# Performance work log

Measured on AMD Instinct MI355X. Metric: run time of the kernel, lower is better.

The kernel has to match this reference:

```python
import jax, jax.numpy as jnp
import numpy as np

N_NODES = 50000
N_EDGES = 400000


def setup_inputs() -> dict:
    key = jax.random.key(0)
    k1, k2, k3, k4 = jax.random.split(key, 4)
    in_feat = jax.random.normal(k1, (2, 64, 4, N_NODES), dtype=jnp.float32)
    src = jax.random.randint(k2, (N_EDGES,), 0, N_NODES, dtype=jnp.int32)
    dst = jax.random.randint(k3, (N_EDGES,), 0, N_NODES, dtype=jnp.int32)
    W = jax.random.normal(k4, (64, 64), dtype=jnp.float32) * (1.0 / 8.0)
    b = jnp.zeros((64,), dtype=jnp.float32)
    return {"in_feat": in_feat, "src": src, "dst": dst, "W": W, "b": b}


def reference(in_feat, src, dst, W, b):
    # in_feat: (B, h, T, N). Net permutation [3,1,2,0] then [0,3,2,1] == [3,0,2,1]
    x = jnp.transpose(in_feat, (3, 0, 2, 1))  # (N, B, T, h) -- node-major for GraphConv
    N = x.shape[0]
    ones_e = jnp.ones(src.shape[0], dtype=x.dtype)
    deg_out = jnp.clip(jax.ops.segment_sum(ones_e, src, num_segments=N), 1.0)
    deg_in = jnp.clip(jax.ops.segment_sum(ones_e, dst, num_segments=N), 1.0)
    # DGL GraphConv, norm='both', in_feats == out_feats -> aggregate then matmul
    x = x * jax.lax.rsqrt(deg_out)[:, None, None, None]
    agg = jax.ops.segment_sum(x[src], dst, num_segments=N)  # (N, B, T, h)
    agg = agg * jax.lax.rsqrt(deg_in)[:, None, None, None]
    h = jnp.einsum('nbth,hf->nbtf', agg, W) + b
    h = jax.nn.relu(h)
    # inverse permutation [0,3,2,1] then [3,1,2,0] == transpose(h, (1,3,2,0))
    out = jnp.transpose(h, (1, 3, 2, 0))  # (B, h, T, N)
    return jax.nn.relu(out)
```

## Files before the change

kernel.cpp:

```cpp
#include <hip/hip_runtime.h>
#include <hip/hip_fp16.h>


typedef _Float16 half8 __attribute__((ext_vector_type(8)));
typedef float f32x4 __attribute__((ext_vector_type(4)));

extern "C" __global__ void k_deg(const int* __restrict__ src, const int* __restrict__ dst,
                                 int* __restrict__ deg_out, int* __restrict__ deg_in, int E) {
  int e = blockIdx.x * blockDim.x + threadIdx.x;
  if (e < E) {
    atomicAdd(&deg_out[src[e]], 1);
    atomicAdd(&deg_in[dst[e]], 1);
  }
}

extern "C" __global__ __launch_bounds__(256) void k_scan1(const int* __restrict__ deg_in,
                                                          const int* __restrict__ deg_out,
                                                          int* __restrict__ bsum,
                                                          float* __restrict__ rs_out,
                                                          float* __restrict__ rs_in, int N) {
  __shared__ int red[256];
  int tid = threadIdx.x;
  int i = blockIdx.x * 256 + tid;
  int di = (i < N) ? deg_in[i] : 0;
  red[tid] = di;
  if (i < N) {
    int a = deg_out[i] > 1 ? deg_out[i] : 1;
    int b = di > 1 ? di : 1;
    rs_out[i] = rsqrtf((float)a);
    rs_in[i]  = rsqrtf((float)b);
  }
  __syncthreads();
  #pragma unroll
  for (int off = 128; off > 0; off >>= 1) {
    if (tid < off) red[tid] += red[tid + off];
    __syncthreads();
  }
  if (tid == 0) bsum[blockIdx.x] = red[0];
}

extern "C" __global__ __launch_bounds__(256) void k_scan3(const int* __restrict__ deg,
                                                          const int* __restrict__ bsum,
                                                          int* __restrict__ offs,
                                                          int* __restrict__ cursor,
                                                          int M, int N) {
  __shared__ int sc[256];
  __shared__ int bs[256];
  int tid = threadIdx.x;

  int bv = (tid < M) ? bsum[tid] : 0;
  bs[tid] = bv;
  __syncthreads();
  #pragma unroll
  for (int off = 1; off < 256; off <<= 1) {
    int t = bs[tid];
    if (tid >= off) t += bs[tid - off];
    __syncthreads();
    bs[tid] = t;
    __syncthreads();
  }
  int boff = (blockIdx.x > 0) ? bs[blockIdx.x - 1] : 0;
  if (blockIdx.x == 0 && tid == 0) offs[N] = bs[255];

  int i = blockIdx.x * 256 + tid;
  int v = (i < N) ? deg[i] : 0;
  sc[tid] = v;
  __syncthreads();
  #pragma unroll
  for (int off = 1; off < 256; off <<= 1) {
    int t = sc[tid];
    if (tid >= off) t += sc[tid - off];
    __syncthreads();
    sc[tid] = t;
    __syncthreads();
  }
  if (i < N) {
    int o = boff + sc[tid] - v;
    offs[i] = o;
    cursor[i] = o;
  }
}

extern "C" __global__ void k_scatter(const int* __restrict__ src, const int* __restrict__ dst,
                                     int* __restrict__ cursor,
                                     int* __restrict__ csr_src, int E) {
  int e = blockIdx.x * blockDim.x + threadIdx.x;
  if (e < E) {
    int pos = atomicAdd(&cursor[dst[e]], 1);
    csr_src[pos] = src[e];
  }
}

extern "C" __global__ __launch_bounds__(128) void k_transform(
    const float* __restrict__ in_feat, const float* __restrict__ W,
    const float* __restrict__ rs_out, __half* __restrict__ y, int N) {
  __shared__ __half ytile[16][264];
  int tid = threadIdx.x;
  int wave = tid >> 6, l = tid & 63;
  int col = l & 15;
  int kg  = l >> 4;
  int n0 = blockIdx.x * 16;
  int btbase = blockIdx.y * 4 + wave * 2;

  half8 wf[4][2];
  #pragma unroll
  for (int ft = 0; ft < 4; ++ft)
    #pragma unroll
    for (int ks = 0; ks < 2; ++ks)
      #pragma unroll
      for (int j = 0; j < 8; ++j)
        wf[ft][ks][j] = (_Float16)W[(ks * 32 + kg * 8 + j) * 64 + ft * 16 + col];

  int nA = n0 + col;
  bool okA = (nA < N);
  float rs = okA ? rs_out[nA] : 0.0f;
  size_t hs = (size_t)4 * (size_t)N;

  float c0[8], c1[8], nx0[8], nx1[8];
  {
    int bt = btbase, b = bt >> 2, t = bt & 3;
    const float* xp = in_feat + (size_t)(b * 256 + t) * (size_t)N + nA;
    #pragma unroll
    for (int j = 0; j < 8; ++j) c0[j] = okA ? xp[(size_t)(kg * 8 + j) * hs] : 0.0f;
    #pragma unroll
    for (int j = 0; j < 8; ++j) c1[j] = okA ? xp[(size_t)(32 + kg * 8 + j) * hs] : 0.0f;
  }

  #pragma unroll
  for (int p = 0; p < 2; ++p) {
    if (p == 0) {
      int bt = btbase + 1, b = bt >> 2, t = bt & 3;
      const float* xp = in_feat + (size_t)(b * 256 + t) * (size_t)N + nA;
      #pragma unroll
      for (int j = 0; j < 8; ++j) nx0[j] = okA ? xp[(size_t)(kg * 8 + j) * hs] : 0.0f;
      #pragma unroll
      for (int j = 0; j < 8; ++j) nx1[j] = okA ? xp[(size_t)(32 + kg * 8 + j) * hs] : 0.0f;
    }
    int btloc = wave * 2 + p;

    half8 a0, a1;
    #pragma unroll
    for (int j = 0; j < 8; ++j) {
      a0[j] = (_Float16)(c0[j] * rs);
      a1[j] = (_Float16)(c1[j] * rs);
    }

    #pragma unroll
    for (int ft = 0; ft < 4; ++ft) {
      f32x4 acc = {0.f, 0.f, 0.f, 0.f};
      acc = __builtin_amdgcn_mfma_f32_16x16x32_f16(a0, wf[ft][0], acc, 0, 0, 0);
      acc = __builtin_amdgcn_mfma_f32_16x16x32_f16(a1, wf[ft][1], acc, 0, 0, 0);
      #pragma unroll
      for (int r = 0; r < 4; ++r)
        ytile[kg * 4 + r][btloc * 64 + ft * 16 + col] = __float2half(acc[r]);
    }

    if (p == 0) {
      #pragma unroll
      for (int j = 0; j < 8; ++j) { c0[j] = nx0[j]; c1[j] = nx1[j]; }
    }
  }
  __syncthreads();

  int row = tid >> 3, seg = tid & 7;
  int nr = n0 + row;
  if (nr < N) {
    const uint4* lp = (const uint4*)&ytile[row][0];
    uint4* gp = (uint4*)(y + (size_t)nr * 512 + blockIdx.y * 256);
    #pragma unroll
    for (int q = 0; q < 4; ++q) gp[seg + q * 8] = lp[seg + q * 8];
  }
}

extern "C" __global__ __launch_bounds__(512) void k_aggregate(
    const __half* __restrict__ y, const int* __restrict__ offs,
    const int* __restrict__ csr_src, const float* __restrict__ rs_in,
    const float* __restrict__ bvec, float* __restrict__ out, int N) {
  __shared__ float agg[16 * 513];
  int tid = threadIdx.x;
  int lane = tid & 63, wave = tid >> 6;
  int n0 = blockIdx.x * 16;

#define ACC_EDGE(s)                                                          \
  {                                                                          \
    const uint2* rp = (const uint2*)(y + (size_t)(s) * 512);                 \
    uint2 ua = rp[lane];                                                     \
    uint2 ub = rp[64 + lane];                                                \
    float2 f;                                                                \
    f = __half22float2(*(const __half2*)&ua.x); accA.x += f.x; accA.y += f.y;\
    f = __half22float2(*(const __half2*)&ua.y); accA.z += f.x; accA.w += f.y;\
    f = __half22float2(*(const __half2*)&ub.x); accB.x += f.x; accB.y += f.y;\
    f = __half22float2(*(const __half2*)&ub.y); accB.z += f.x; accB.w += f.y;\
  }

  #pragma unroll
  for (int k = 0; k < 2; ++k) {
    int nl = k * 8 + wave;
    int n = n0 + nl;
    float4 accA = {0.f, 0.f, 0.f, 0.f};
    float4 accB = {0.f, 0.f, 0.f, 0.f};
    if (n < N) {
      int j0 = offs[n], j1 = offs[n + 1];
      for (int base = j0; base < j1; base += 64) {
        int idxv = csr_src[base + lane];
        int m = j1 - base; if (m > 64) m = 64;
        int e = 0;
        for (; e + 3 < m; e += 4) {
          int s0 = __builtin_amdgcn_readlane(idxv, e);
          int s1 = __builtin_amdgcn_readlane(idxv, e + 1);
          int s2 = __builtin_amdgcn_readlane(idxv, e + 2);
          int s3 = __builtin_amdgcn_readlane(idxv, e + 3);
          ACC_EDGE(s0); ACC_EDGE(s1); ACC_EDGE(s2); ACC_EDGE(s3);
        }
        for (; e < m; ++e) {
          int s0 = __builtin_amdgcn_readlane(idxv, e);
          ACC_EDGE(s0);
        }
      }
    }
    *(float4*)&agg[nl * 513 + lane * 4] = accA;
    *(float4*)&agg[nl * 513 + 256 + lane * 4] = accB;
  }
#undef ACC_EDGE
  __syncthreads();

  int nl = tid & 15;
  int r0 = tid >> 4;
  int n = n0 + nl;
  float rs = (n < N) ? rs_in[n] : 0.0f;
  #pragma unroll 4
  for (int it = 0; it < 16; ++it) {
    int c = it * 32 + r0;
    float v = agg[nl * 513 + c];
    int f = c & 63, bt = c >> 6;
    int b = bt >> 2, t = bt & 3;
    v = v * rs + bvec[f];
    v = fmaxf(v, 0.0f);
    if (n < N)
      __builtin_nontemporal_store(v, &out[(size_t)((b * 64 + f) * 4 + t) * (size_t)N + n]);
  }
}

extern "C" void kernel_launch(void* const* d_in, const int* in_sizes, int n_in,
                              void* d_out, int out_size, void* d_ws, size_t ws_size,
                              hipStream_t stream) {
  const float* in_feat = (const float*)d_in[0];
  const int*   src     = (const int*)d_in[1];
  const int*   dst     = (const int*)d_in[2];
  const float* W       = (const float*)d_in[3];
  const float* bvec    = (const float*)d_in[4];
  float* out = (float*)d_out;

  int N = in_sizes[0] / 512;
  int E = in_sizes[1];

  int A  = (N + 64) & ~63;
  int EA = (E + 63) & ~63;
  int M  = (N + 255) / 256;

  int*   deg_out_i = (int*)d_ws;
  int*   deg_in_i  = deg_out_i + A;
  int*   cursor    = deg_in_i + A;
  int*   offs      = cursor + A;
  int*   bsum      = offs + A;
  float* rs_out    = (float*)(bsum + 256);
  float* rs_in     = rs_out + A;
  int*   csr_src   = (int*)(rs_in + A);
  __half* y        = (__half*)(csr_src + EA);

  hipMemsetAsync(deg_out_i, 0, (size_t)(2 * A) * sizeof(int), stream);
  hipLaunchKernelGGL(k_deg, dim3((E + 255) / 256), dim3(256), 0, stream,
                     src, dst, deg_out_i, deg_in_i, E);
  hipLaunchKernelGGL(k_scan1, dim3(M), dim3(256), 0, stream,
                     deg_in_i, deg_out_i, bsum, rs_out, rs_in, N);
  hipLaunchKernelGGL(k_scan3, dim3(M), dim3(256), 0, stream,
                     deg_in_i, bsum, offs, cursor, M, N);
  hipLaunchKernelGGL(k_scatter, dim3((E + 255) / 256), dim3(256), 0, stream,
                     src, dst, cursor, csr_src, E);
  hipLaunchKernelGGL(k_transform, dim3((N + 15) / 16, 2), dim3(128), 0, stream,
                     in_feat, W, rs_out, y, N);
  hipLaunchKernelGGL(k_aggregate, dim3((N + 15) / 16), dim3(512), 0, stream,
                     y, offs, csr_src, rs_in, bvec, out, N);
}
```

Measured before the change: 180.0 us.

## Stage transform input through LDS with float4 coalesced loads over 64-node tiles

Restructures k_transform so each 256-thread block covers 64 nodes. Input features are loaded as float4 vectors along the node dimension, scaled, converted to half and staged in shared memory. MFMA operands are then read from that LDS tile, replacing the old 16-node strided scalar loads and their register double-buffering. The grid changes to (N/64, 4) with two bt slices per block. The aim is wider, better-coalesced global reads, at the cost of extra barriers and LDS traffic and no overlap of the next load with compute.

```diff
diff --git a/kernel.cpp b/kernel.cpp
--- a/kernel.cpp
+++ b/kernel.cpp
@@ -91,16 +91,16 @@
   }
 }
 
-extern "C" __global__ __launch_bounds__(128) void k_transform(
+extern "C" __global__ __launch_bounds__(256) void k_transform(
     const float* __restrict__ in_feat, const float* __restrict__ W,
     const float* __restrict__ rs_out, __half* __restrict__ y, int N) {
-  __shared__ __half ytile[16][264];
+  __shared__ __half xs[64][68];
+  __shared__ __half yt[64][72];
   int tid = threadIdx.x;
   int wave = tid >> 6, l = tid & 63;
   int col = l & 15;
   int kg  = l >> 4;
-  int n0 = blockIdx.x * 16;
-  int btbase = blockIdx.y * 4 + wave * 2;
+  int n0 = blockIdx.x * 64;
 
   half8 wf[4][2];
   #pragma unroll
@@ -111,39 +111,49 @@
       for (int j = 0; j < 8; ++j)
         wf[ft][ks][j] = (_Float16)W[(ks * 32 + kg * 8 + j) * 64 + ft * 16 + col];
 
-  int nA = n0 + col;
-  bool okA = (nA < N);
-  float rs = okA ? rs_out[nA] : 0.0f;
-  size_t hs = (size_t)4 * (size_t)N;
-
-  float c0[8], c1[8], nx0[8], nx1[8];
-  {
-    int bt = btbase, b = bt >> 2, t = bt & 3;
-    const float* xp = in_feat + (size_t)(b * 256 + t) * (size_t)N + nA;
-    #pragma unroll
-    for (int j = 0; j < 8; ++j) c0[j] = okA ? xp[(size_t)(kg * 8 + j) * hs] : 0.0f;
-    #pragma unroll
-    for (int j = 0; j < 8; ++j) c1[j] = okA ? xp[(size_t)(32 + kg * 8 + j) * hs] : 0.0f;
-  }
+  int hq = tid >> 4, nq = tid & 15;
+  int nb = n0 + 4 * nq;
+  float rs4[4];
+  #pragma unroll
+  for (int c = 0; c < 4; ++c)
+    rs4[c] = (nb + c < N) ? rs_out[nb + c] : 0.0f;
+  bool full4 = (nb + 3 < N);
 
   #pragma unroll
   for (int p = 0; p < 2; ++p) {
-    if (p == 0) {
-      int bt = btbase + 1, b = bt >> 2, t = bt & 3;
-      const float* xp = in_feat + (size_t)(b * 256 + t) * (size_t)N + nA;
-      #pragma unroll
-      for (int j = 0; j < 8; ++j) nx0[j] = okA ? xp[(size_t)(kg * 8 + j) * hs] : 0.0f;
-      #pragma unroll
-      for (int j = 0; j < 8; ++j) nx1[j] = okA ? xp[(size_t)(32 + kg * 8 + j) * hs] : 0.0f;
-    }
-    int btloc = wave * 2 + p;
-
+    int bt = blockIdx.y * 2 + p;
+    int b = bt >> 2, t = bt & 3;
+    const float* xbase = in_feat + (size_t)(b * 256 + t) * (size_t)N;
+
+    __syncthreads();
+    #pragma unroll
+    for (int i = 0; i < 4; ++i) {
+      int h = hq + 16 * i;
+      const float* xp = xbase + (size_t)h * 4 * (size_t)N + nb;
+      float v0 = 0.f, v1 = 0.f, v2 = 0.f, v3 = 0.f;
+      if (full4) {
+        float4 v = *(const float4*)xp;
+        v0 = v.x; v1 = v.y; v2 = v.z; v3 = v.w;
+      } else {
+        if (nb < N)     v0 = xp[0];
+        if (nb + 1 < N) v1 = xp[1];
+        if (nb + 2 < N) v2 = xp[2];
+      }
+      __half2 h0 = __float22half2_rn(make_float2(v0 * rs4[0], v1 * rs4[1]));
+      __half2 h1 = __float22half2_rn(make_float2(v2 * rs4[2], v3 * rs4[3]));
+      uint2 u;
+      u.x = *(unsigned int*)&h0;
+      u.y = *(unsigned int*)&h1;
+      *(uint2*)&xs[h][4 * nq] = u;
+    }
+    __syncthreads();
+
+    int nloc = 16 * wave + col;
     half8 a0, a1;
     #pragma unroll
-    for (int j = 0; j < 8; ++j) {
-      a0[j] = (_Float16)(c0[j] * rs);
-      a1[j] = (_Float16)(c1[j] * rs);
-    }
+    for (int j = 0; j < 8; ++j) a0[j] = (_Float16)xs[kg * 8 + j][nloc];
+    #pragma unroll
+    for (int j = 0; j < 8; ++j) a1[j] = (_Float16)xs[32 + kg * 8 + j][nloc];
 
     #pragma unroll
     for (int ft = 0; ft < 4; ++ft) {
@@ -152,23 +162,17 @@
       acc = __builtin_amdgcn_mfma_f32_16x16x32_f16(a1, wf[ft][1], acc, 0, 0, 0);
       #pragma unroll
       for (int r = 0; r < 4; ++r)
-        ytile[kg * 4 + r][btloc * 64 + ft * 16 + col] = __float2half(acc[r]);
-    }
-
-    if (p == 0) {
-      #pragma unroll
-      for (int j = 0; j < 8; ++j) { c0[j] = nx0[j]; c1[j] = nx1[j]; }
-    }
-  }
-  __syncthreads();
-
-  int row = tid >> 3, seg = tid & 7;
-  int nr = n0 + row;
-  if (nr < N) {
-    const uint4* lp = (const uint4*)&ytile[row][0];
-    uint4* gp = (uint4*)(y + (size_t)nr * 512 + blockIdx.y * 256);
-    #pragma unroll
-    for (int q = 0; q < 4; ++q) gp[seg + q * 8] = lp[seg + q * 8];
+        yt[16 * wave + kg * 4 + r][ft * 16 + col] = __float2half(acc[r]);
+    }
+    __syncthreads();
+
+    int node = tid >> 2, sg = tid & 3;
+    int nr = n0 + node;
+    if (nr < N) {
+      uint4* gp = (uint4*)(y + (size_t)nr * 512 + bt * 64);
+      gp[sg]     = *(const uint4*)&yt[node][sg * 8];
+      gp[sg + 4] = *(const uint4*)&yt[node][(sg + 4) * 8];
+    }
   }
 }
 
@@ -257,6 +261,7 @@
   int A  = (N + 64) & ~63;
   int EA = (E + 63) & ~63;
   int M  = (N + 255) / 256;
+  int GX = (N + 63) / 64;
 
   int*   deg_out_i = (int*)d_ws;
   int*   deg_in_i  = deg_out_i + A;
@@ -277,7 +282,7 @@
                      deg_in_i, bsum, offs, cursor, M, N);
   hipLaunchKernelGGL(k_scatter, dim3((E + 255) / 256), dim3(256), 0, stream,
                      src, dst, cursor, csr_src, E);
-  hipLaunchKernelGGL(k_transform, dim3((N + 15) / 16, 2), dim3(128), 0, stream,
+  hipLaunchKernelGGL(k_transform, dim3(GX, 4), dim3(256), 0, stream,
                      in_feat, W, rs_out, y, N);
   hipLaunchKernelGGL(k_aggregate, dim3((N + 15) / 16), dim3(512), 0, stream,
                      y, offs, csr_src, rs_in, bvec, out, N);
```

Result: faster. 173.6 us (median of 2 runs) (-3.6%).
